# Kernel tuning notes

Hardware: AMD Instinct MI355X
Metric: run time of the kernel (lower is better)

## Reference

```python
import jax, jax.numpy as jnp
import numpy as np

NUM_EXPERTS = 8

def setup_inputs() -> dict:
    key = jax.random.key(0)
    x = jax.random.normal(key, (8192, NUM_EXPERTS, 1024), dtype=jnp.float32)
    return {"x": x}

def reference(x):
    # Gram-Schmidt orthonormalization of the num_experts vectors per batch row.
    # x: [B, E, D] -> basis: [B, E, D] with orthonormal rows along E.
    b0 = x[:, 0, :]
    b0 = b0 / jnp.linalg.norm(b0, axis=-1, keepdims=True)
    basis = b0[:, None, :]  # [B, 1, D]
    num_experts = x.shape[1]
    for i in range(1, num_experts):
        v = x[:, i, :]  # [B, D]
        # coefficients of v on current orthonormal basis: [B, k]
        coeff = jnp.einsum('bd,bkd->bk', v, basis)
        w = v - jnp.einsum('bk,bkd->bd', coeff, basis)
        wn = w / jnp.linalg.norm(w, axis=-1, keepdims=True)
        basis = jnp.concatenate([basis, wn[:, None, :]], axis=1)
    return basis
```

## Files before the change

### kernel.cpp

```cpp
#include <hip/hip_runtime.h>


constexpr int NE      = 8;
constexpr int DIM     = 1024;
constexpr int THREADS = 256;
constexpr int VPT     = DIM / THREADS;
constexpr int NWAVES  = THREADS / 64;
constexpr int NPAIR   = NE * (NE + 1) / 2;

__global__ __launch_bounds__(THREADS, 4) void gs_chol_kernel(const float* __restrict__ x,
                                                             float* __restrict__ out) {
    const int b    = blockIdx.x;
    const int tid  = threadIdx.x;
    const int lane = tid & 63;
    const int wid  = tid >> 6;
    const size_t base = (size_t)b * NE * DIM;

    float v[NE][VPT];
    #pragma unroll
    for (int e = 0; e < NE; ++e) {
        const float4 t = *reinterpret_cast<const float4*>(x + base + (size_t)e * DIM + tid * VPT);
        v[e][0] = t.x; v[e][1] = t.y; v[e][2] = t.z; v[e][3] = t.w;
    }

    float p[NPAIR];
    #pragma unroll
    for (int i = 0; i < NE; ++i) {
        #pragma unroll
        for (int k = 0; k <= i; ++k) {
            const int d = i * (i + 1) / 2 + k;
            float s = v[i][0] * v[k][0];
            #pragma unroll
            for (int j = 1; j < VPT; ++j) s = fmaf(v[i][j], v[k][j], s);
            p[d] = s;
        }
    }

    #pragma unroll
    for (int d = 0; d < NPAIR; ++d) {
        float s = p[d];
        #pragma unroll
        for (int o = 32; o > 0; o >>= 1) s += __shfl_xor(s, o);
        p[d] = s;
    }

    __shared__ alignas(16) float part[NPAIR][NWAVES];
    if (lane == 0) {
        #pragma unroll
        for (int d = 0; d < NPAIR; ++d) part[d][wid] = p[d];
    }
    __syncthreads();

    float L[NPAIR];
    float rinv[NE];
    #pragma unroll
    for (int i = 0; i < NE; ++i) {
        #pragma unroll
        for (int k = 0; k <= i; ++k) {
            const int d = i * (i + 1) / 2 + k;
            const float4 g4 = *reinterpret_cast<const float4*>(&part[d][0]);
            float s = (g4.x + g4.y) + (g4.z + g4.w);
            #pragma unroll
            for (int m = 0; m < k; ++m)
                s = fmaf(-L[i * (i + 1) / 2 + m], L[k * (k + 1) / 2 + m], s);
            if (k == i) {
                const float li = sqrtf(s);
                L[d]    = li;
                rinv[i] = 1.0f / li;
            } else {
                L[d] = s * rinv[k];
            }
        }
    }

    #pragma unroll
    for (int i = 0; i < NE; ++i) {
        #pragma unroll
        for (int j = 0; j < VPT; ++j) {
            float w = v[i][j];
            #pragma unroll
            for (int k = 0; k < i; ++k)
                w = fmaf(-L[i * (i + 1) / 2 + k], v[k][j], w);
            v[i][j] = w * rinv[i];
        }
        float4 t; t.x = v[i][0]; t.y = v[i][1]; t.z = v[i][2]; t.w = v[i][3];
        *reinterpret_cast<float4*>(out + base + (size_t)i * DIM + tid * VPT) = t;
    }
}

extern "C" void kernel_launch(void* const* d_in, const int* in_sizes, int n_in,
                              void* d_out, int out_size, void* d_ws, size_t ws_size,
                              hipStream_t stream) {
    const float* x = (const float*)d_in[0];
    float* out = (float*)d_out;
    const int batches = in_sizes[0] / (NE * DIM);
    gs_chol_kernel<<<batches, THREADS, 0, stream>>>(x, out);
}
```

Baseline: 437.2 us.

## Assign one wavefront per batch row to drop shared-memory reduction and block barrier

Each 64-lane wavefront now handles a whole batch row, with 16 elements per lane per expert instead of 4. The Gram dot products are reduced entirely with wave shuffles, so the shared-memory partial array and the __syncthreads are gone. In exchange each thread holds 128 values plus the Gram terms in registers, the launch-bounds occupancy hint falls from 4 to 2 blocks, and the grid shrinks by 4x. Because each wave holds a full row independently, memory-level parallelism now depends on how many waves stay resident under the higher register pressure. The grid assumes the batch count divides evenly by 4.

```diff
diff --git a/kernel.cpp b/kernel.cpp
--- a/kernel.cpp
+++ b/kernel.cpp
@@ -4,23 +4,27 @@
 constexpr int NE      = 8;
 constexpr int DIM     = 1024;
 constexpr int THREADS = 256;
-constexpr int VPT     = DIM / THREADS;
-constexpr int NWAVES  = THREADS / 64;
+constexpr int WPB     = THREADS / 64;
+constexpr int EPT     = DIM / 64;
 constexpr int NPAIR   = NE * (NE + 1) / 2;
 
-__global__ __launch_bounds__(THREADS, 4) void gs_chol_kernel(const float* __restrict__ x,
+__global__ __launch_bounds__(THREADS, 2) void gs_wave_kernel(const float* __restrict__ x,
                                                              float* __restrict__ out) {
-    const int b    = blockIdx.x;
-    const int tid  = threadIdx.x;
-    const int lane = tid & 63;
-    const int wid  = tid >> 6;
-    const size_t base = (size_t)b * NE * DIM;
+    const int lane = threadIdx.x & 63;
+    const int wid  = threadIdx.x >> 6;
+    const size_t batch = (size_t)blockIdx.x * WPB + wid;
+    const float* xb = x   + batch * NE * DIM + lane * 4;
+    float*       ob = out + batch * NE * DIM + lane * 4;
 
-    float v[NE][VPT];
+    float v[NE][EPT];
     #pragma unroll
     for (int e = 0; e < NE; ++e) {
-        const float4 t = *reinterpret_cast<const float4*>(x + base + (size_t)e * DIM + tid * VPT);
-        v[e][0] = t.x; v[e][1] = t.y; v[e][2] = t.z; v[e][3] = t.w;
+        #pragma unroll
+        for (int q = 0; q < 4; ++q) {
+            const float4 t = *reinterpret_cast<const float4*>(xb + e * DIM + q * 256);
+            v[e][q * 4 + 0] = t.x; v[e][q * 4 + 1] = t.y;
+            v[e][q * 4 + 2] = t.z; v[e][q * 4 + 3] = t.w;
+        }
     }
 
     float p[NPAIR];
@@ -28,11 +32,10 @@
     for (int i = 0; i < NE; ++i) {
         #pragma unroll
         for (int k = 0; k <= i; ++k) {
-            const int d = i * (i + 1) / 2 + k;
-            float s = v[i][0] * v[k][0];
+            float s = 0.0f;
             #pragma unroll
-            for (int j = 1; j < VPT; ++j) s = fmaf(v[i][j], v[k][j], s);
-            p[d] = s;
+            for (int j = 0; j < EPT; ++j) s = fmaf(v[i][j], v[k][j], s);
+            p[i * (i + 1) / 2 + k] = s;
         }
     }
 
@@ -44,31 +47,22 @@
         p[d] = s;
     }
 
-    __shared__ alignas(16) float part[NPAIR][NWAVES];
-    if (lane == 0) {
-        #pragma unroll
-        for (int d = 0; d < NPAIR; ++d) part[d][wid] = p[d];
-    }
-    __syncthreads();
-
     float L[NPAIR];
     float rinv[NE];
     #pragma unroll
     for (int i = 0; i < NE; ++i) {
         #pragma unroll
         for (int k = 0; k <= i; ++k) {
-            const int d = i * (i + 1) / 2 + k;
-            const float4 g4 = *reinterpret_cast<const float4*>(&part[d][0]);
-            float s = (g4.x + g4.y) + (g4.z + g4.w);
+            float s = p[i * (i + 1) / 2 + k];
             #pragma unroll
             for (int m = 0; m < k; ++m)
                 s = fmaf(-L[i * (i + 1) / 2 + m], L[k * (k + 1) / 2 + m], s);
             if (k == i) {
                 const float li = sqrtf(s);
-                L[d]    = li;
+                L[i * (i + 1) / 2 + i] = li;
                 rinv[i] = 1.0f / li;
             } else {
-                L[d] = s * rinv[k];
+                L[i * (i + 1) / 2 + k] = s * rinv[k];
             }
         }
     }
@@ -76,15 +70,20 @@
     #pragma unroll
     for (int i = 0; i < NE; ++i) {
         #pragma unroll
-        for (int j = 0; j < VPT; ++j) {
+        for (int j = 0; j < EPT; ++j) {
             float w = v[i][j];
             #pragma unroll
             for (int k = 0; k < i; ++k)
                 w = fmaf(-L[i * (i + 1) / 2 + k], v[k][j], w);
             v[i][j] = w * rinv[i];
         }
-        float4 t; t.x = v[i][0]; t.y = v[i][1]; t.z = v[i][2]; t.w = v[i][3];
-        *reinterpret_cast<float4*>(out + base + (size_t)i * DIM + tid * VPT) = t;
+        #pragma unroll
+        for (int q = 0; q < 4; ++q) {
+            float4 t;
+            t.x = v[i][q * 4 + 0]; t.y = v[i][q * 4 + 1];
+            t.z = v[i][q * 4 + 2]; t.w = v[i][q * 4 + 3];
+            *reinterpret_cast<float4*>(ob + i * DIM + q * 256) = t;
+        }
     }
 }
 
@@ -94,5 +93,5 @@
     const float* x = (const float*)d_in[0];
     float* out = (float*)d_out;
     const int batches = in_sizes[0] / (NE * DIM);
-    gs_chol_kernel<<<batches, THREADS, 0, stream>>>(x, out);
+    gs_wave_kernel<<<batches / WPB, THREADS, 0, stream>>>(x, out);
 }
```

Result: no change. 433.1 us (-0.9%).
